# Optimization experiments

Measured on AMD Instinct MI355X. Metric: run time of the kernel, lower is better.

The kernel has to match this reference:

```python
import jax, jax.numpy as jnp
import numpy as np

NUM_HEADS = 12
D_MODEL = 768


def setup_inputs() -> dict:
    key = jax.random.key(0)
    ks = jax.random.split(key, 5)
    B, S = 2, 2048
    x = jax.random.normal(ks[0], (B, S, D_MODEL), dtype=jnp.float32)
    # additive causal mask: 0 on/below diagonal, -1e9 above
    causal = jnp.tril(jnp.ones((S, S), dtype=bool))
    attn_mask = jnp.where(causal, 0.0, -1e9).astype(jnp.float32)
    lim_in = 1.0 / np.sqrt(D_MODEL)
    w_in = jax.random.uniform(ks[1], (3 * D_MODEL, D_MODEL), jnp.float32, -lim_in, lim_in)
    b_in = jax.random.uniform(ks[2], (3 * D_MODEL,), jnp.float32, -lim_in, lim_in)
    w_out = jax.random.uniform(ks[3], (D_MODEL, D_MODEL), jnp.float32, -lim_in, lim_in)
    b_out = jax.random.uniform(ks[4], (D_MODEL,), jnp.float32, -lim_in, lim_in)
    return {"x": x, "attn_mask": attn_mask, "w_in": w_in, "b_in": b_in,
            "w_out": w_out, "b_out": b_out}


def reference(x, attn_mask, w_in, b_in, w_out, b_out):
    B, S, d_model = x.shape
    H = NUM_HEADS
    d_head = d_model // H
    # fused QKV projection (torch Linear: x @ W^T + b)
    projected = x @ w_in.T + b_in                      # [B, S, 3*d_model]
    # faithful reinterpretation as in the source: row-major view to
    # [B*H, S, d_head, 3] (q/k/v interleaved on last axis, heads folded
    # across the flat buffer). No 1/sqrt(d_head) scaling in the source.
    qkv = projected.reshape(B * H, S, d_head, 3)
    q = qkv[..., 0]                                    # [B*H, S, d_head]
    k = qkv[..., 1]
    v = qkv[..., 2]
    logits = jnp.einsum('nsd,ntd->nst', q, k) + attn_mask  # [B*H, S, S]
    weights = jax.nn.softmax(logits, axis=-1)          # dropout_p = 0
    heads = jnp.einsum('nst,ntd->nsd', weights, v)     # [B*H, S, d_head]
    out = heads.reshape(B, H, S, d_head).transpose(0, 2, 1, 3).reshape(B, S, d_model)
    return out @ w_out.T + b_out
```

## Files before the change

kernel.cpp:

```cpp
#include <hip/hip_runtime.h>
#include <hip/hip_bf16.h>
#include <stdint.h>

typedef __attribute__((ext_vector_type(8))) short bf16x8;
typedef __attribute__((ext_vector_type(4))) float f32x4;
typedef __attribute__((ext_vector_type(16))) float f32x16;
typedef __attribute__((ext_vector_type(4))) unsigned short u16x4;

__device__ __forceinline__ unsigned short f2bf(float f) {
    unsigned int u = __builtin_bit_cast(unsigned int, f);
    u = (u + 0x7fffu + ((u >> 16) & 1u)) >> 16;
    return (unsigned short)u;
}

__device__ __forceinline__ void gl2lds16(const void* g, void* l) {
    __builtin_amdgcn_global_load_lds(
        (const __attribute__((address_space(1))) unsigned int*)g,
        (__attribute__((address_space(3))) unsigned int*)l, 16, 0, 0);
}

__global__ __launch_bounds__(256)
void cvt_all(const float* __restrict__ x, const float* __restrict__ wi, const float* __restrict__ wo,
             unsigned short* __restrict__ xb, unsigned short* __restrict__ wb1,
             unsigned short* __restrict__ wb2) {
    const int bid = blockIdx.x;
    const float* src; unsigned short* dst; int i;
    if (bid < 3072)      { src = x;  dst = xb;  i = bid * 256 + threadIdx.x; }
    else if (bid < 4800) { src = wi; dst = wb1; i = (bid - 3072) * 256 + threadIdx.x; }
    else                 { src = wo; dst = wb2; i = (bid - 4800) * 256 + threadIdx.x; }
    float4 v = reinterpret_cast<const float4*>(src)[i];
    union { unsigned short u[4]; uint2 p; } o;
    o.u[0] = f2bf(v.x); o.u[1] = f2bf(v.y); o.u[2] = f2bf(v.z); o.u[3] = f2bf(v.w);
    reinterpret_cast<uint2*>(dst)[i] = o.p;
}

__global__ __launch_bounds__(256)
void gemm_bt(const unsigned short* __restrict__ A, const unsigned short* __restrict__ B,
             const float* __restrict__ bias, int M, int N, int K, int mode,
             unsigned short* __restrict__ bf_out, float* __restrict__ f32_out) {
    __shared__ unsigned short Al[128][32];
    __shared__ unsigned short Bl[128][32];
    const int tid = threadIdx.x;
    const int wid = tid >> 6, lane = tid & 63;
    const int m0 = blockIdx.y * 128, n0 = blockIdx.x * 128;
    const int wm = (wid >> 1) * 64, wn = (wid & 1) * 64;
    const int lrow = lane & 15;
    f32x4 acc[4][4];
#pragma unroll
    for (int a = 0; a < 4; a++)
#pragma unroll
        for (int b = 0; b < 4; b++) acc[a][b] = f32x4{0.f, 0.f, 0.f, 0.f};
    for (int k0 = 0; k0 < K; k0 += 32) {
#pragma unroll
        for (int i = 0; i < 2; i++) {
            const int fb_base = i * 256 + (tid & ~63);
            const int fb = i * 256 + tid;
            const int row = fb >> 2, blk = fb & 3;
            const int sb = blk ^ ((row >> 1) & 3);
            gl2lds16(&A[(size_t)(m0 + row) * K + k0 + sb * 8], (char*)&Al[0][0] + fb_base * 16);
            gl2lds16(&B[(size_t)(n0 + row) * K + k0 + sb * 8], (char*)&Bl[0][0] + fb_base * 16);
        }
        __syncthreads();
        bf16x8 af[4], bfr[4];
#pragma unroll
        for (int i = 0; i < 4; i++) {
            const int row = wm + i*16 + lrow;
            const int g = (lane >> 4) ^ ((row >> 1) & 3);
            af[i] = *reinterpret_cast<const bf16x8*>(&Al[row][g * 8]);
        }
#pragma unroll
        for (int i = 0; i < 4; i++) {
            const int row = wn + i*16 + lrow;
            const int g = (lane >> 4) ^ ((row >> 1) & 3);
            bfr[i] = *reinterpret_cast<const bf16x8*>(&Bl[row][g * 8]);
        }
#pragma unroll
        for (int mi = 0; mi < 4; mi++)
#pragma unroll
            for (int ni = 0; ni < 4; ni++)
                acc[mi][ni] = __builtin_amdgcn_mfma_f32_16x16x32_bf16(af[mi], bfr[ni], acc[mi][ni], 0, 0, 0);
        __syncthreads();
    }
    const int rb = (lane >> 4) * 4;
#pragma unroll
    for (int mi = 0; mi < 4; mi++)
#pragma unroll
        for (int ni = 0; ni < 4; ni++) {
            int cc = n0 + wn + ni*16 + lrow;
            float bv = bias[cc];
#pragma unroll
            for (int i = 0; i < 4; i++) {
                int r = m0 + wm + mi*16 + rb + i;
                float v = acc[mi][ni][i] + bv;
                if (mode == 0) {
                    bf_out[(size_t)r * N + cc] = f2bf(v);
                } else {
                    f32_out[(size_t)r * N + cc] = v;
                }
            }
        }
}

__global__ __launch_bounds__(256)
void deint(const unsigned short* __restrict__ P, unsigned short* __restrict__ qkv,
           unsigned int* __restrict__ ctr) {
    __shared__ unsigned short L[6144];
    const int tid = threadIdx.x;
    if (blockIdx.x == 0 && tid == 0) *ctr = 0u;
    const size_t base = (size_t)blockIdx.x * 6144;
#pragma unroll
    for (int s = 0; s < 3; ++s) {
        int idx = (s * 256 + tid) * 8;
        *reinterpret_cast<bf16x8*>(&L[idx]) = *reinterpret_cast<const bf16x8*>(&P[base + idx]);
    }
    __syncthreads();
    const int u0 = blockIdx.x * 32;
    const int n = u0 >> 11, t0 = u0 & 2047;
#pragma unroll
    for (int s = 0; s < 2; ++s) {
        int ww = s * 256 + tid;
        int j = ww >> 8;
        int cc = (ww & 255) >> 3;
        int o = ww & 7;
        bf16x8 vv;
#pragma unroll
        for (int q = 0; q < 8; ++q) vv[q] = (short)L[cc * 192 + 3 * (o * 8 + q) + j];
        *reinterpret_cast<bf16x8*>(&qkv[(size_t)j * 3145728 + (size_t)(u0 + cc) * 64 + o * 8]) = vv;
    }
    {
        int d = tid >> 2, g = tid & 3;
        bf16x8 vv;
#pragma unroll
        for (int e = 0; e < 8; ++e) vv[e] = (short)L[(g * 8 + e) * 192 + 3 * d + 2];
        *reinterpret_cast<bf16x8*>(&qkv[6291456 + (size_t)n * 131072 + (size_t)d * 2048 + t0 + g * 8]) = vv;
    }
}

#define ANITEMS 576
__global__ __launch_bounds__(256, 2)
void attn_fwd(const unsigned short* __restrict__ qkv, unsigned short* __restrict__ Hb,
              float* __restrict__ Op, float2* __restrict__ Ml, unsigned int* __restrict__ ctr) {
    __shared__ unsigned short Kl[2][64][64];
    __shared__ unsigned short Vl[2][64][64];
    __shared__ int s_item;
    static const unsigned char CLS[24] = {
        30,31,14,28,29,26,27,12,24,25,22,23,10,20,21,18,19,8,16,17,6,4,2,0};
    const int tid = threadIdx.x, w = tid >> 6, lane = tid & 63;
    const int l31 = lane & 31, l7 = lane & 7, hi = lane >> 5;

    for (;;) {
        __syncthreads();
        if (tid == 0) s_item = (int)atomicAdd(ctr, 1u);
        __syncthreads();
        const int item = s_item;
        if (item >= ANITEMS) break;
        const int c = item / 24;
        const int n = item - c * 24;
        const int v = CLS[c];
        const int qb = v >> 1, ch = v & 1;
        const int split = (qb >= 8) ? 1 : 0;
        const int tstart = split ? ch * (qb + 1) : 0;
        const int nt = split ? (qb + 1) : (2 * qb + 2);
        const int q0w = qb * 128 + w * 32;
        const int q_lane = q0w + l31;
        const unsigned short* Qg = qkv + (size_t)n * 131072;
        const unsigned short* Kg = qkv + 3145728 + (size_t)n * 131072;
        const unsigned short* Vg = qkv + 6291456 + (size_t)n * 131072;

        bf16x8 qf[4];
#pragma unroll
        for (int s = 0; s < 4; s++)
            qf[s] = *reinterpret_cast<const bf16x8*>(&Qg[(size_t)q_lane * 64 + 16*s + 8*hi]);

        f32x16 oa[2];
#pragma unroll
        for (int dt = 0; dt < 2; dt++)
#pragma unroll
            for (int r = 0; r < 16; r++) oa[dt][r] = 0.f;
        float m_run = -3.0e38f, l_run = 0.f;

        auto stage = [&](int buf, int gt) {
            const int tb = gt * 64;
#pragma unroll
            for (int i = 0; i < 2; i++) {
                const int fb_base = i * 256 + (tid & ~63);
                const int fb = i * 256 + tid;
                const int t = fb >> 3, p = fb & 7;
                gl2lds16(&Kg[(size_t)(tb + t) * 64 + ((p ^ (t & 7)) << 3)],
                         (char*)&Kl[buf][0][0] + fb_base * 16);
                gl2lds16(&Vg[(size_t)t * 2048 + tb + ((p ^ (t & 7)) << 3)],
                         (char*)&Vl[buf][0][0] + fb_base * 16);
            }
        };

        stage(0, tstart);
        int cur = 0;
        for (int tt = 0; tt < nt; ++tt) {
            __syncthreads();
            const int t0 = (tstart + tt) * 64;
            if (tt + 1 < nt) stage(cur ^ 1, tstart + tt + 1);
            if (t0 <= q0w + 31) {
                f32x16 sa[2];
#pragma unroll
                for (int t2 = 0; t2 < 2; t2++)
#pragma unroll
                    for (int r = 0; r < 16; r++) sa[t2][r] = 0.f;
#pragma unroll
                for (int t2 = 0; t2 < 2; t2++)
#pragma unroll
                    for (int s = 0; s < 4; s++) {
                        bf16x8 kf = *reinterpret_cast<const bf16x8*>(
                            &Kl[cur][32*t2 + l31][((2*s + hi) ^ l7) << 3]);
                        sa[t2] = __builtin_amdgcn_mfma_f32_32x32x16_bf16(kf, qf[s], sa[t2], 0, 0, 0);
                    }
                if (t0 + 63 > q0w) {
#pragma unroll
                    for (int t2 = 0; t2 < 2; t2++)
#pragma unroll
                        for (int r = 0; r < 16; r++) {
                            int t = t0 + 32*t2 + (r & 3) + 8*(r >> 2) + 4*hi;
                            if (t > q_lane) sa[t2][r] = -1e30f;
                        }
                }
                float mx = sa[0][0];
#pragma unroll
                for (int t2 = 0; t2 < 2; t2++)
#pragma unroll
                    for (int r = 0; r < 16; r++) mx = fmaxf(mx, sa[t2][r]);
                mx = fmaxf(mx, __shfl_xor(mx, 32));
                float mn = fmaxf(m_run, mx);
                float alpha = __expf(m_run - mn);
                m_run = mn;
                float rs = 0.f;
#pragma unroll
                for (int t2 = 0; t2 < 2; t2++)
#pragma unroll
                    for (int r = 0; r < 16; r++) {
                        float p = __expf(sa[t2][r] - mn);
                        sa[t2][r] = p;
                        rs += p;
                    }
                rs += __shfl_xor(rs, 32);
                l_run = l_run * alpha + rs;
#pragma unroll
                for (int dt = 0; dt < 2; dt++)
#pragma unroll
                    for (int r = 0; r < 16; r++) oa[dt][r] *= alpha;
                bf16x8 pfrag[4];
#pragma unroll
                for (int t2 = 0; t2 < 2; t2++) {
                    unsigned int pk[8];
#pragma unroll
                    for (int k2 = 0; k2 < 8; k2++) {
                        float lo = sa[t2][2*k2], hi2 = sa[t2][2*k2 + 1];
                        unsigned int r;
                        asm("v_cvt_pk_bf16_f32 %0, %1, %2" : "=v"(r) : "v"(lo), "v"(hi2));
                        pk[k2] = r;
                    }
                    asm("v_permlane32_swap_b32 %0, %1" : "+v"(pk[0]), "+v"(pk[2]));
                    asm("v_permlane32_swap_b32 %0, %1" : "+v"(pk[1]), "+v"(pk[3]));
                    asm("v_permlane32_swap_b32 %0, %1" : "+v"(pk[4]), "+v"(pk[6]));
                    asm("v_permlane32_swap_b32 %0, %1" : "+v"(pk[5]), "+v"(pk[7]));
                    union { unsigned int u[4]; bf16x8 v; } f0, f1;
                    f0.u[0] = pk[0]; f0.u[1] = pk[1]; f0.u[2] = pk[2]; f0.u[3] = pk[3];
                    f1.u[0] = pk[4]; f1.u[1] = pk[5]; f1.u[2] = pk[6]; f1.u[3] = pk[7];
                    pfrag[2*t2]     = f0.v;
                    pfrag[2*t2 + 1] = f1.v;
                }
#pragma unroll
                for (int dt = 0; dt < 2; dt++)
#pragma unroll
                    for (int sp = 0; sp < 4; sp++) {
                        bf16x8 vf = *reinterpret_cast<const bf16x8*>(
                            &Vl[cur][32*dt + l31][((2*sp + hi) ^ l7) << 3]);
                        oa[dt] = __builtin_amdgcn_mfma_f32_32x32x16_bf16(vf, pfrag[sp], oa[dt], 0, 0, 0);
                    }
            }
            cur ^= 1;
        }
        const int b = n / 12, h = n - (n / 12) * 12;
        if (!split) {
            const float inv = 1.0f / l_run;
            const size_t rowb = ((size_t)(b * 2048 + q_lane)) * 768 + h * 64;
#pragma unroll
            for (int dt = 0; dt < 2; dt++)
#pragma unroll
                for (int g = 0; g < 4; g++) {
                    u16x4 o4;
#pragma unroll
                    for (int e = 0; e < 4; e++) o4[e] = f2bf(oa[dt][4*g + e] * inv);
                    *reinterpret_cast<u16x4*>(&Hb[rowb + 32*dt + 8*g + 4*hi]) = o4;
                }
        } else {
            const int rr = q_lane - 1024;
            const size_t pbase = ((size_t)(n * 1024 + rr) * 2 + ch) * 64;
#pragma unroll
            for (int dt = 0; dt < 2; dt++)
#pragma unroll
                for (int g = 0; g < 4; g++) {
                    float4 o4;
                    o4.x = oa[dt][4*g + 0]; o4.y = oa[dt][4*g + 1];
                    o4.z = oa[dt][4*g + 2]; o4.w = oa[dt][4*g + 3];
                    *reinterpret_cast<float4*>(&Op[pbase + 32*dt + 8*g + 4*hi]) = o4;
                }
            if (hi == 0) {
                float2 mlv; mlv.x = m_run; mlv.y = l_run;
                Ml[(n * 1024 + rr) * 2 + ch] = mlv;
            }
        }
    }
}

__global__ __launch_bounds__(256)
void attn_combine(const float* __restrict__ Op, const float2* __restrict__ Ml,
                  unsigned short* __restrict__ Hb) {
    const int tid = threadIdx.x;
    const int row = blockIdx.x * 4 + (tid >> 6);
    const int d = tid & 63;
    const int n = row >> 10, r = row & 1023;
    const float2 a = Ml[row * 2 + 0];
    const float2 bml = Ml[row * 2 + 1];
    const float M = fmaxf(a.x, bml.x);
    const float w0 = __expf(a.x - M), w1 = __expf(bml.x - M);
    const float inv = 1.0f / (w0 * a.y + w1 * bml.y);
    const float o = (w0 * Op[(size_t)(row * 2 + 0) * 64 + d] +
                     w1 * Op[(size_t)(row * 2 + 1) * 64 + d]) * inv;
    const int bb = n / 12, h = n - (n / 12) * 12;
    Hb[((size_t)(bb * 2048 + 1024 + r)) * 768 + h * 64 + d] = f2bf(o);
}

extern "C" void kernel_launch(void* const* d_in, const int* in_sizes, int n_in,
                              void* d_out, int out_size, void* d_ws, size_t ws_size,
                              hipStream_t stream) {
    const float* x     = (const float*)d_in[0];
    const float* w_in  = (const float*)d_in[2];
    const float* b_in  = (const float*)d_in[3];
    const float* w_out = (const float*)d_in[4];
    const float* b_out = (const float*)d_in[5];
    float* out = (float*)d_out;

    unsigned short* xb   = (unsigned short*)d_ws;
    unsigned short* wb1  = xb  + 3145728;
    unsigned short* wb2  = wb1 + 1769472;
    unsigned short* proj = wb2 + 589824;
    unsigned short* qkvb = proj + 9437184;
    unsigned short* hb   = qkvb + 9437184;
    unsigned int* ctr = (unsigned int*)xb;
    float2*       Ml  = (float2*)(xb + 64);
    float*        Op  = (float*)proj;

    cvt_all<<<5376, 256, 0, stream>>>(x, w_in, w_out, xb, wb1, wb2);

    gemm_bt<<<dim3(2304 / 128, 4096 / 128), 256, 0, stream>>>(
        xb, wb1, b_in, 4096, 2304, 768, 0, proj, nullptr);

    deint<<<1536, 256, 0, stream>>>(proj, qkvb, ctr);

    attn_fwd<<<512, 256, 0, stream>>>(qkvb, hb, Op, Ml, ctr);

    attn_combine<<<6144, 256, 0, stream>>>(Op, Ml, hb);

    gemm_bt<<<dim3(768 / 128, 4096 / 128), 256, 0, stream>>>(
        hb, wb2, b_out, 4096, 768, 768, 1, nullptr, out);
}
```

Before: 186.4 us.

## Double-buffer GEMM staging, retile out-proj, and split attention KV into 8-tile chunks

The GEMM becomes a template with double-buffered LDS staging, so the next K slice loads while MFMAs run on the current one, and one barrier per iteration is dropped. The output projection switches to 128x64 tiles to launch more blocks. Attention work items are re-split so that any query block with more than 8 KV tiles is cut into chunks of at most 8 tiles, up to 4 per row. This raises the item count from 576 to 960, and the combine kernel merges a variable number of partials. The cost is more partial-output traffic and a larger combine pass, with Op and Ml moved to a dedicated workspace region.

```diff
diff --git a/kernel.cpp b/kernel.cpp
--- a/kernel.cpp
+++ b/kernel.cpp
@@ -34,63 +34,79 @@
     reinterpret_cast<uint2*>(dst)[i] = o.p;
 }
 
+template<int BM, int BN>
 __global__ __launch_bounds__(256)
 void gemm_bt(const unsigned short* __restrict__ A, const unsigned short* __restrict__ B,
              const float* __restrict__ bias, int M, int N, int K, int mode,
              unsigned short* __restrict__ bf_out, float* __restrict__ f32_out) {
-    __shared__ unsigned short Al[128][32];
-    __shared__ unsigned short Bl[128][32];
+    __shared__ unsigned short Al[2][BM][32];
+    __shared__ unsigned short Bl[2][BN][32];
     const int tid = threadIdx.x;
     const int wid = tid >> 6, lane = tid & 63;
-    const int m0 = blockIdx.y * 128, n0 = blockIdx.x * 128;
-    const int wm = (wid >> 1) * 64, wn = (wid & 1) * 64;
+    const int m0 = blockIdx.y * BM, n0 = blockIdx.x * BN;
+    const int wm = (wid >> 1) * (BM / 2), wn = (wid & 1) * (BN / 2);
     const int lrow = lane & 15;
-    f32x4 acc[4][4];
-#pragma unroll
-    for (int a = 0; a < 4; a++)
-#pragma unroll
-        for (int b = 0; b < 4; b++) acc[a][b] = f32x4{0.f, 0.f, 0.f, 0.f};
-    for (int k0 = 0; k0 < K; k0 += 32) {
-#pragma unroll
-        for (int i = 0; i < 2; i++) {
-            const int fb_base = i * 256 + (tid & ~63);
+    constexpr int MR = BM / 32, NR = BN / 32;
+    f32x4 acc[MR][NR];
+#pragma unroll
+    for (int a = 0; a < MR; a++)
+#pragma unroll
+        for (int b = 0; b < NR; b++) acc[a][b] = f32x4{0.f, 0.f, 0.f, 0.f};
+
+    auto stage = [&](int buf, int k0) {
+#pragma unroll
+        for (int i = 0; i < BM / 64; i++) {
             const int fb = i * 256 + tid;
             const int row = fb >> 2, blk = fb & 3;
             const int sb = blk ^ ((row >> 1) & 3);
-            gl2lds16(&A[(size_t)(m0 + row) * K + k0 + sb * 8], (char*)&Al[0][0] + fb_base * 16);
-            gl2lds16(&B[(size_t)(n0 + row) * K + k0 + sb * 8], (char*)&Bl[0][0] + fb_base * 16);
-        }
+            gl2lds16(&A[(size_t)(m0 + row) * K + k0 + sb * 8],
+                     (char*)&Al[buf][0][0] + (i * 256 + (tid & ~63)) * 16);
+        }
+#pragma unroll
+        for (int i = 0; i < BN / 64; i++) {
+            const int fb = i * 256 + tid;
+            const int row = fb >> 2, blk = fb & 3;
+            const int sb = blk ^ ((row >> 1) & 3);
+            gl2lds16(&B[(size_t)(n0 + row) * K + k0 + sb * 8],
+                     (char*)&Bl[buf][0][0] + (i * 256 + (tid & ~63)) * 16);
+        }
+    };
+
+    stage(0, 0);
+    const int NS = K >> 5;
+    for (int it = 0; it < NS; ++it) {
         __syncthreads();
-        bf16x8 af[4], bfr[4];
-#pragma unroll
-        for (int i = 0; i < 4; i++) {
-            const int row = wm + i*16 + lrow;
+        const int cur = it & 1;
+        if (it + 1 < NS) stage(cur ^ 1, (it + 1) << 5);
+        bf16x8 af[MR], bfr[NR];
+#pragma unroll
+        for (int i = 0; i < MR; i++) {
+            const int row = wm + i * 16 + lrow;
             const int g = (lane >> 4) ^ ((row >> 1) & 3);
-            af[i] = *reinterpret_cast<const bf16x8*>(&Al[row][g * 8]);
-        }
-#pragma unroll
-        for (int i = 0; i < 4; i++) {
-            const int row = wn + i*16 + lrow;
+            af[i] = *reinterpret_cast<const bf16x8*>(&Al[cur][row][g * 8]);
+        }
+#pragma unroll
+        for (int i = 0; i < NR; i++) {
+            const int row = wn + i * 16 + lrow;
             const int g = (lane >> 4) ^ ((row >> 1) & 3);
-            bfr[i] = *reinterpret_cast<const bf16x8*>(&Bl[row][g * 8]);
-        }
-#pragma unroll
-        for (int mi = 0; mi < 4; mi++)
-#pragma unroll
-            for (int ni = 0; ni < 4; ni++)
+            bfr[i] = *reinterpret_cast<const bf16x8*>(&Bl[cur][row][g * 8]);
+        }
+#pragma unroll
+        for (int mi = 0; mi < MR; mi++)
+#pragma unroll
+            for (int ni = 0; ni < NR; ni++)
                 acc[mi][ni] = __builtin_amdgcn_mfma_f32_16x16x32_bf16(af[mi], bfr[ni], acc[mi][ni], 0, 0, 0);
-        __syncthreads();
     }
     const int rb = (lane >> 4) * 4;
 #pragma unroll
-    for (int mi = 0; mi < 4; mi++)
-#pragma unroll
-        for (int ni = 0; ni < 4; ni++) {
-            int cc = n0 + wn + ni*16 + lrow;
+    for (int mi = 0; mi < MR; mi++)
+#pragma unroll
+        for (int ni = 0; ni < NR; ni++) {
+            int cc = n0 + wn + ni * 16 + lrow;
             float bv = bias[cc];
 #pragma unroll
             for (int i = 0; i < 4; i++) {
-                int r = m0 + wm + mi*16 + rb + i;
+                int r = m0 + wm + mi * 16 + rb + i;
                 float v = acc[mi][ni][i] + bv;
                 if (mode == 0) {
                     bf_out[(size_t)r * N + cc] = f2bf(v);
@@ -136,15 +152,16 @@
     }
 }
 
-#define ANITEMS 576
+#define ANITEMS 960
 __global__ __launch_bounds__(256, 2)
 void attn_fwd(const unsigned short* __restrict__ qkv, unsigned short* __restrict__ Hb,
               float* __restrict__ Op, float2* __restrict__ Ml, unsigned int* __restrict__ ctr) {
     __shared__ unsigned short Kl[2][64][64];
     __shared__ unsigned short Vl[2][64][64];
     __shared__ int s_item;
-    static const unsigned char CLS[24] = {
-        30,31,14,28,29,26,27,12,24,25,22,23,10,20,21,18,19,8,16,17,6,4,2,0};
+    static const unsigned char CLS[40] = {
+        60,61,62,63, 56,57,58, 52,53,54, 48,49,50, 44,45,46, 40,41, 36,37,
+        32,33, 28,29, 24, 20, 16, 12, 59,42,25,8, 55,38,21,4, 51,34,17,0};
     const int tid = threadIdx.x, w = tid >> 6, lane = tid & 63;
     const int l31 = lane & 31, l7 = lane & 7, hi = lane >> 5;
 
@@ -157,10 +174,12 @@
         const int c = item / 24;
         const int n = item - c * 24;
         const int v = CLS[c];
-        const int qb = v >> 1, ch = v & 1;
-        const int split = (qb >= 8) ? 1 : 0;
-        const int tstart = split ? ch * (qb + 1) : 0;
-        const int nt = split ? (qb + 1) : (2 * qb + 2);
+        const int qb = v >> 2, ch = v & 3;
+        const int ntfull = 2 * qb + 2;
+        const int nch = (ntfull + 7) >> 3;
+        const int split = (nch > 1) ? 1 : 0;
+        const int tstart = ch * 8;
+        const int nt = (ntfull - tstart < 8) ? (ntfull - tstart) : 8;
         const int q0w = qb * 128 + w * 32;
         const int q_lane = q0w + l31;
         const unsigned short* Qg = qkv + (size_t)n * 131072;
@@ -292,8 +311,8 @@
                     *reinterpret_cast<u16x4*>(&Hb[rowb + 32*dt + 8*g + 4*hi]) = o4;
                 }
         } else {
-            const int rr = q_lane - 1024;
-            const size_t pbase = ((size_t)(n * 1024 + rr) * 2 + ch) * 64;
+            const int rr = q_lane - 512;
+            const size_t pbase = ((size_t)(n * 1536 + rr) * 4 + ch) * 64;
 #pragma unroll
             for (int dt = 0; dt < 2; dt++)
 #pragma unroll
@@ -305,7 +324,7 @@
                 }
             if (hi == 0) {
                 float2 mlv; mlv.x = m_run; mlv.y = l_run;
-                Ml[(n * 1024 + rr) * 2 + ch] = mlv;
+                Ml[(n * 1536 + rr) * 4 + ch] = mlv;
             }
         }
     }
@@ -314,19 +333,22 @@
 __global__ __launch_bounds__(256)
 void attn_combine(const float* __restrict__ Op, const float2* __restrict__ Ml,
                   unsigned short* __restrict__ Hb) {
-    const int tid = threadIdx.x;
-    const int row = blockIdx.x * 4 + (tid >> 6);
-    const int d = tid & 63;
-    const int n = row >> 10, r = row & 1023;
-    const float2 a = Ml[row * 2 + 0];
-    const float2 bml = Ml[row * 2 + 1];
-    const float M = fmaxf(a.x, bml.x);
-    const float w0 = __expf(a.x - M), w1 = __expf(bml.x - M);
-    const float inv = 1.0f / (w0 * a.y + w1 * bml.y);
-    const float o = (w0 * Op[(size_t)(row * 2 + 0) * 64 + d] +
-                     w1 * Op[(size_t)(row * 2 + 1) * 64 + d]) * inv;
+    const int idx = blockIdx.x * 256 + threadIdx.x;
+    const int d = idx & 63, rowg = idx >> 6;
+    const int n = rowg / 1536, rr = rowg - n * 1536;
+    const int qb = (512 + rr) >> 7;
+    const int nch = (2 * qb + 9) >> 3;
+    float M = -3.0e38f;
+    for (int c = 0; c < nch; c++) M = fmaxf(M, Ml[rowg * 4 + c].x);
+    float lsum = 0.f, osum = 0.f;
+    for (int c = 0; c < nch; c++) {
+        const float2 ml = Ml[rowg * 4 + c];
+        const float wgt = __expf(ml.x - M);
+        lsum += wgt * ml.y;
+        osum += wgt * Op[(size_t)(rowg * 4 + c) * 64 + d];
+    }
     const int bb = n / 12, h = n - (n / 12) * 12;
-    Hb[((size_t)(bb * 2048 + 1024 + r)) * 768 + h * 64 + d] = f2bf(o);
+    Hb[((size_t)(bb * 2048 + 512 + rr)) * 768 + h * 64 + d] = f2bf(osum / lsum);
 }
 
 extern "C" void kernel_launch(void* const* d_in, const int* in_sizes, int n_in,
@@ -345,21 +367,21 @@
     unsigned short* proj = wb2 + 589824;
     unsigned short* qkvb = proj + 9437184;
     unsigned short* hb   = qkvb + 9437184;
+    float*        Op  = (float*)(hb + 3145728);
+    float2*       Ml  = (float2*)(Op + 9437184);
     unsigned int* ctr = (unsigned int*)xb;
-    float2*       Ml  = (float2*)(xb + 64);
-    float*        Op  = (float*)proj;
 
     cvt_all<<<5376, 256, 0, stream>>>(x, w_in, w_out, xb, wb1, wb2);
 
-    gemm_bt<<<dim3(2304 / 128, 4096 / 128), 256, 0, stream>>>(
+    gemm_bt<128,128><<<dim3(18, 32), 256, 0, stream>>>(
         xb, wb1, b_in, 4096, 2304, 768, 0, proj, nullptr);
 
     deint<<<1536, 256, 0, stream>>>(proj, qkvb, ctr);
 
     attn_fwd<<<512, 256, 0, stream>>>(qkvb, hb, Op, Ml, ctr);
 
-    attn_combine<<<6144, 256, 0, stream>>>(Op, Ml, hb);
-
-    gemm_bt<<<dim3(768 / 128, 4096 / 128), 256, 0, stream>>>(
+    attn_combine<<<9216, 256, 0, stream>>>(Op, Ml, hb);
+
+    gemm_bt<128,64><<<dim3(12, 32), 256, 0, stream>>>(
         hb, wb2, b_out, 4096, 768, 768, 1, nullptr, out);
 }
```

Result: no change. 186.6 us (+0.1%).
